# Kernel tuning notes

Hardware: AMD Instinct MI355X
Metric: run time of the kernel (lower is better)

## Reference

```python
import jax, jax.numpy as jnp
import numpy as np

B, S, E, H, D, W = 2, 4096, 512, 8, 64, 512
NUM_BUCKETS, MAX_DISTANCE = 32, 128  # hardcoded in get_relative_positions for 't5'
NEG_INF = -1e30


def _t5_bucket_causal(relative_position):
    """T5 relative position bucketing, unidirectional (causal)."""
    n = jnp.maximum(-relative_position, 0)
    max_exact = NUM_BUCKETS // 2
    is_small = n < max_exact
    nf = jnp.maximum(n.astype(jnp.float32), 1.0)
    val_if_large = max_exact + (
        jnp.log(nf / max_exact) / np.log(MAX_DISTANCE / max_exact)
        * (NUM_BUCKETS - max_exact)
    ).astype(jnp.int32)
    val_if_large = jnp.minimum(val_if_large, NUM_BUCKETS - 1)
    return jnp.where(is_small, n, val_if_large)


def setup_inputs() -> dict:
    key = jax.random.key(0)
    ks = jax.random.split(key, 7)
    scale = 1.0 / np.sqrt(E)  # keep logits in a sane range
    return {
        'xs': jax.random.normal(ks[0], (B, S, E), jnp.float32),
        'prev_k': jax.random.normal(ks[1], (B, W, H, D), jnp.float32),
        'prev_v': jax.random.normal(ks[2], (B, W, H, D), jnp.float32),
        'w_q': jax.random.normal(ks[3], (E, H, D), jnp.float32) * scale,
        'w_k': jax.random.normal(ks[4], (E, H, D), jnp.float32) * scale,
        'w_v': jax.random.normal(ks[5], (E, H, D), jnp.float32) * scale,
        'rel_bias': jax.random.normal(ks[6], (H, NUM_BUCKETS), jnp.float32),
    }


def reference(xs, prev_k, prev_v, w_q, w_k, w_v, rel_bias):
    nw = S // W  # number of windows
    # kvq projections; queries pre-scaled by 1/sqrt(head_size)
    q = jnp.einsum('bse,ehd->bshd', xs, w_q) * (1.0 / np.sqrt(D))
    k = jnp.einsum('bse,ehd->bshd', xs, w_k)
    v = jnp.einsum('bse,ehd->bshd', xs, w_v)
    qw = q.reshape(B, nw, W, H, D)
    kw = k.reshape(B, nw, W, H, D)
    vw = v.reshape(B, nw, W, H, D)
    # Transformer-XL sliding window: keys for window i = [window i-1 keys ; window i keys]
    k_prev = jnp.concatenate([prev_k[:, None], kw[:, :-1]], axis=1)  # (B,nw,W,H,D)
    v_prev = jnp.concatenate([prev_v[:, None], vw[:, :-1]], axis=1)
    k2 = jnp.concatenate([k_prev, kw], axis=2)  # (B,nw,2W,H,D)
    v2 = jnp.concatenate([v_prev, vw], axis=2)
    # T5 relative position bias and causal mask (num_queries=W, num_keys=2W)
    ctx = jnp.arange(W)[:, None] + W          # query absolute position in key frame
    mem = jnp.arange(2 * W)[None, :]
    relpos = mem - ctx                        # (W, 2W), key - query
    bias = rel_bias[:, _t5_bucket_causal(relpos)]  # (H, W, 2W)
    # causal + window mask: key j attends iff i < j <= i+W (each query sees exactly W keys)
    mask = (relpos <= 0) & (relpos > -W)
    # attention per window
    scores = jnp.einsum('bnqhd,bnkhd->bnhqk', qw, k2)  # (B,nw,H,W,2W)
    scores = scores + bias[None, None]
    scores = jnp.where(mask[None, None, None], scores, NEG_INF)
    probs = jax.nn.softmax(scores, axis=-1)
    attn = jnp.einsum('bnhqk,bnkhd->bnqhd', probs, v2)
    attn_ys = attn.reshape(B, S, H, D)
    # next_kvi cache = last window's keys/values
    next_k = kw[:, -1]
    next_v = vw[:, -1]
    return attn_ys, next_k, next_v
```

## Files before the change

### kernel.cpp

```cpp
#include <hip/hip_runtime.h>
#include <hip/hip_bf16.h>
#include <math.h>

#define B_ 2
#define S_ 4096
#define H_ 8
#define D_ 64
#define W_ 512

#define MASKV -1e30f

typedef float f32x4 __attribute__((ext_vector_type(4)));
typedef short s16x4 __attribute__((ext_vector_type(4)));
typedef short s16x8 __attribute__((ext_vector_type(8)));
typedef unsigned int u32;
typedef __attribute__((address_space(1))) const u32 as1_u32;
typedef __attribute__((address_space(3))) u32 as3_u32;

__device__ inline short f2bf(float f) {
    unsigned u = __builtin_bit_cast(unsigned, f);
    unsigned r = (u + 0x7FFFu + ((u >> 16) & 1u)) >> 16;
    return (short)r;
}
__device__ inline s16x8 pack8(f32x4 a, f32x4 b) {
    s16x8 r;
    r[0]=f2bf(a[0]); r[1]=f2bf(a[1]); r[2]=f2bf(a[2]); r[3]=f2bf(a[3]);
    r[4]=f2bf(b[0]); r[5]=f2bf(b[1]); r[6]=f2bf(b[2]); r[7]=f2bf(b[3]);
    return r;
}
__device__ __forceinline__ void gl_lds16(const void* g, void* l) {
    __builtin_amdgcn_global_load_lds((as1_u32*)(unsigned long long)g,
                                     (as3_u32*)(u32)(unsigned long long)l,
                                     16, 0, 0);
}
__device__ __forceinline__ void drain_vmem() {
    asm volatile("s_waitcnt vmcnt(0)" ::: "memory");
}

__global__ __launch_bounds__(256, 4)
void prep_kernel(const float* __restrict__ xs, const float* __restrict__ pk,
                 const float* __restrict__ pv, const float* __restrict__ wq,
                 const float* __restrict__ wk, const float* __restrict__ wv,
                 short* __restrict__ xsbf, short* __restrict__ pkbf,
                 short* __restrict__ vbt, short* __restrict__ wt)
{
    __shared__ char smem[17408];
    const int bid = blockIdx.x;
    const int tid = threadIdx.x;

    if (bid < 2304) {
        size_t i8 = ((size_t)bid * 256 + tid) * 8;
        const float* src; short* dst; size_t off;
        if (i8 < 4194304) { src = xs; dst = xsbf; off = i8; }
        else              { src = pk; dst = pkbf; off = i8 - 4194304; }
        f32x4 a = *(const f32x4*)(src + off);
        f32x4 b = *(const f32x4*)(src + off + 4);
        *(s16x8*)(dst + off) = pack8(a, b);
    } else if (bid < 2432) {
        short (*st)[72] = (short(*)[72])smem;
        const int b2 = bid - 2304;
        const int jt = b2 & 7, h = (b2 >> 3) & 7, b = b2 >> 6;
        const int jj0 = jt * 64;
        {
            int kk = tid >> 2, d0 = (tid & 3) * 16;
            const float* src = pv + (((size_t)(b * 512 + jj0 + kk)) * 8 + h) * 64 + d0;
            f32x4 x0 = *(const f32x4*)(src);
            f32x4 x1 = *(const f32x4*)(src + 4);
            f32x4 x2 = *(const f32x4*)(src + 8);
            f32x4 x3 = *(const f32x4*)(src + 12);
            *(s16x8*)&st[kk][d0]     = pack8(x0, x1);
            *(s16x8*)&st[kk][d0 + 8] = pack8(x2, x3);
        }
        __syncthreads();
        {
            int dd = tid >> 2, k0 = (tid & 3) * 16;
            s16x8 o0, o1;
            #pragma unroll
            for (int t = 0; t < 8; ++t) { o0[t] = st[k0 + t][dd]; o1[t] = st[k0 + 8 + t][dd]; }
            short* dst = vbt + (size_t)(h * 64 + dd) * 9216 + b * 4608 + jj0 + k0;
            *(s16x8*)dst = o0;
            *(s16x8*)(dst + 8) = o1;
        }
    } else {
        float (*st)[68] = (float(*)[68])smem;
        const int t2 = bid - 2432;
        const int k0 = (t2 & 7) * 64;
        const int nt = t2 >> 3;
        const int z  = nt >> 3;
        const int n0 = (nt & 7) * 64;
        const float* wz = (z == 0) ? wq : (z == 1) ? wk : wv;
        const float scale = (z == 0) ? 0.125f : 1.0f;
        {
            int kk = tid >> 4, nn = (tid & 15) * 4;
            #pragma unroll
            for (int it = 0; it < 4; ++it) {
                f32x4 x = *(const f32x4*)(wz + (size_t)(k0 + kk + it * 16) * 512 + n0 + nn);
                *(f32x4*)&st[kk + it * 16][nn] = x;
            }
        }
        __syncthreads();
        {
            int nn2 = tid >> 2, kseg = (tid & 3) * 16;
            s16x8 o0, o1;
            #pragma unroll
            for (int j = 0; j < 8; ++j) o0[j] = f2bf(st[kseg + j][nn2] * scale);
            #pragma unroll
            for (int j = 0; j < 8; ++j) o1[j] = f2bf(st[kseg + 8 + j][nn2] * scale);
            short* dst = wt + (size_t)(z * 512 + n0 + nn2) * 512 + k0 + kseg;
            *(s16x8*)(dst) = o0;
            *(s16x8*)(dst + 8) = o1;
        }
    }
}

__global__ __launch_bounds__(256, 4)
void proj_kernel(const short* __restrict__ xsbf, const short* __restrict__ wt,
                 short* __restrict__ qkbf, short* __restrict__ vbt,
                 float* __restrict__ out)
{
    __shared__ short Xs[128][64];
    __shared__ short Ws[128][64];

    const int tid = threadIdx.x;
    const int m0  = blockIdx.x * 128;
    const int n0  = blockIdx.y * 128;
    const int z   = n0 >> 9;
    const int ln0 = n0 & 511;
    const int wave = tid >> 6, lane = tid & 63;
    const int wq = (wave & 1) * 64;
    const int wx = (wave >> 1) * 64;
    const int lr = lane & 15, quad = lane >> 4;

    f32x4 acc[4][4] = {};

    const int r8  = lane >> 3;
    const int gr  = lane & 7;

    for (int k0 = 0; k0 < 512; k0 += 64) {
        #pragma unroll
        for (int i = 0; i < 4; ++i) {
            int row = 32 * wave + 8 * i + r8;
            int gs  = gr ^ (row & 7);
            gl_lds16(xsbf + (size_t)(m0 + row) * 512 + k0 + gs * 8, &Xs[32 * wave + 8 * i][0]);
            gl_lds16(wt   + (size_t)(n0 + row) * 512 + k0 + gs * 8, &Ws[32 * wave + 8 * i][0]);
        }
        drain_vmem();
        __syncthreads();
        #pragma unroll
        for (int ks = 0; ks < 2; ++ks) {
            s16x8 af[4], bf[4];
            #pragma unroll
            for (int ta = 0; ta < 4; ++ta) {
                int R = wq + ta * 16 + lr;
                af[ta] = *(const s16x8*)&Ws[R][(((ks * 4 + quad) ^ (R & 7)) * 8)];
            }
            #pragma unroll
            for (int tb = 0; tb < 4; ++tb) {
                int R = wx + tb * 16 + lr;
                bf[tb] = *(const s16x8*)&Xs[R][(((ks * 4 + quad) ^ (R & 7)) * 8)];
            }
            #pragma unroll
            for (int ta = 0; ta < 4; ++ta)
                #pragma unroll
                for (int tb = 0; tb < 4; ++tb)
                    acc[ta][tb] = __builtin_amdgcn_mfma_f32_16x16x32_bf16(
                        af[ta], bf[tb], acc[ta][tb], 0, 0, 0);
        }
        __syncthreads();
    }

    #pragma unroll
    for (int ta = 0; ta < 4; ++ta)
        #pragma unroll
        for (int tb = 0; tb < 4; ++tb) {
            int m  = m0 + wx + tb * 16 + lr;
            int ln = ln0 + wq + ta * 16 + quad * 4;
            int bb = m >> 12, seq = m & 4095;
            if (z < 2) {
                short* base = qkbf + (size_t)z * ((size_t)8192 * 512);
                s16x4 o;
                o[0] = f2bf(acc[ta][tb][0]); o[1] = f2bf(acc[ta][tb][1]);
                o[2] = f2bf(acc[ta][tb][2]); o[3] = f2bf(acc[ta][tb][3]);
                *(s16x4*)(base + (size_t)m * 512 + ln) = o;
                if (z == 1 && seq >= 3584) {
                    float* dst = out + 4194304 + ((size_t)(bb * 512 + seq - 3584)) * 512 + ln;
                    *(f32x4*)dst = acc[ta][tb];
                }
            } else {
                size_t col = (size_t)bb * 4608 + 512 + seq;
                #pragma unroll
                for (int g = 0; g < 4; ++g)
                    vbt[(size_t)(ln + g) * 9216 + col] = f2bf(acc[ta][tb][g]);
                if (seq >= 3584) {
                    float* dst = out + 4194304 + 524288 + ((size_t)(bb * 512 + seq - 3584)) * 512 + ln;
                    *(f32x4*)dst = acc[ta][tb];
                }
            }
        }
}

__global__ __launch_bounds__(512, 4)
void attn_kernel(const short* __restrict__ qkbf, const short* __restrict__ vbt,
                 const short* __restrict__ pkbf, const float* __restrict__ rel_bias,
                 float* __restrict__ out)
{
    __shared__ short k_s[2][64][64];
    __shared__ short vt_s[2][64][64];
    __shared__ short p_s[128][64];
    __shared__ float bias_s[512];

    const short* qb = qkbf;
    const short* kb = qkbf + (size_t)8192 * 512;

    const int bid = blockIdx.x;
    const int qt = bid & 3;
    const int h  = (bid >> 2) & 7;
    const int n  = (bid >> 5) & 7;
    const int b  = bid >> 8;
    const int tid = threadIdx.x;
    const int wave = tid >> 6, lane = tid & 63;
    const int lr = lane & 15, quad = lane >> 4;
    const int q0 = qt * 128;
    const int i0 = q0 + 16 * wave;

    {
        int nd = tid;
        int bucket;
        if (nd < 16) bucket = nd;
        else {
            int vbk = 16 + (int)(log((double)nd * (1.0 / 16.0)) * (16.0 / log(8.0)));
            bucket = vbk < 31 ? vbk : 31;
        }
        bias_s[nd] = rel_bias[h * 32 + bucket];
    }
    const float bias31 = rel_bias[h * 32 + 31];

    s16x8 aq[2];
    {
        const short* src = qb + (size_t)(b * S_ + n * W_ + i0 + lr) * 512 + h * 64 + quad * 8;
        aq[0] = *(const s16x8*)(src);
        aq[1] = *(const s16x8*)(src + 32);
    }

    f32x4 oacc[4] = {};
    float lsum = 0.f;

    const int cmin = (16 * wave) >> 6;
    const int cmax = (16 * wave + 527) >> 6;

    const int r8 = lane >> 3, gr = lane & 7;

    auto issueKV = [&](int c, int pb) {
        int jj = q0 + 64 * c + 8 * wave + r8;
        int p  = n * W_ + jj - W_;
        int gs = gr ^ r8;
        const short* ksrc = (p >= 0)
            ? kb   + ((size_t)(b * S_ + p)) * 512 + h * 64 + gs * 8
            : pkbf + (((size_t)(b * W_ + jj)) * 8 + h) * 64 + gs * 8;
        gl_lds16(ksrc, &k_s[pb][8 * wave][0]);
        int drow = 8 * wave + r8;
        const short* vsrc = vbt + (size_t)(h * 64 + drow) * 9216
                          + b * 4608 + n * W_ + q0 + 64 * c + gs * 8;
        gl_lds16(vsrc, &vt_s[pb][8 * wave][0]);
    };

    issueKV(0, 0);

    for (int c = 0; c < 10; ++c) {
        const int pb = c & 1;
        drain_vmem();
        __syncthreads();
        if (c < 9) issueKV(c + 1, pb ^ 1);
        if (c < cmin || c > cmax) continue;

        f32x4 sacc[4] = {};
        #pragma unroll
        for (int ks = 0; ks < 2; ++ks) {
            s16x8 bk[4];
            #pragma unroll
            for (int tn = 0; tn < 4; ++tn)
                bk[tn] = *(const s16x8*)&k_s[pb][tn * 16 + lr][(((4 * ks + quad) ^ (lr & 7)) * 8)];
            #pragma unroll
            for (int tn = 0; tn < 4; ++tn)
                sacc[tn] = __builtin_amdgcn_mfma_f32_16x16x32_bf16(
                    bk[tn], aq[ks], sacc[tn], 0, 0, 0);
        }

        const int ib = i0 + lr;
        const int jb = q0 + 64 * c;
        if (64 * c - 16 * wave <= 336) {
            #pragma unroll
            for (int tn = 0; tn < 4; ++tn) {
                s16x4 pp;
                #pragma unroll
                for (int rg = 0; rg < 4; ++rg) {
                    int j = jb + tn * 16 + quad * 4 + rg;
                    unsigned dm1 = (unsigned)(j - ib - 1);
                    float sv = (dm1 < 512u) ? (sacc[tn][rg] + bias31) : MASKV;
                    float p = __expf(sv);
                    lsum += p;
                    pp[rg] = f2bf(p);
                }
                int gp = (2 * tn + (quad >> 1)) ^ (lr & 7);
                *(s16x4*)&p_s[16 * wave + lr][gp * 8 + (quad & 1) * 4] = pp;
            }
        } else {
            #pragma unroll
            for (int tn = 0; tn < 4; ++tn) {
                s16x4 pp;
                #pragma unroll
                for (int rg = 0; rg < 4; ++rg) {
                    int j = jb + tn * 16 + quad * 4 + rg;
                    unsigned dm1 = (unsigned)(j - ib - 1);
                    float bias = bias_s[(ib + 512 - j) & 511];
                    float sv = (dm1 < 512u) ? (sacc[tn][rg] + bias) : MASKV;
                    float p = __expf(sv);
                    lsum += p;
                    pp[rg] = f2bf(p);
                }
                int gp = (2 * tn + (quad >> 1)) ^ (lr & 7);
                *(s16x4*)&p_s[16 * wave + lr][gp * 8 + (quad & 1) * 4] = pp;
            }
        }

        asm volatile("s_waitcnt lgkmcnt(0)" ::: "memory");

        #pragma unroll
        for (int ks = 0; ks < 2; ++ks) {
            int gpa = (4 * ks + quad) ^ (lr & 7);
            s16x8 ap = *(const s16x8*)&p_s[16 * wave + lr][gpa * 8];
            s16x8 bv[4];
            #pragma unroll
            for (int tn = 0; tn < 4; ++tn)
                bv[tn] = *(const s16x8*)&vt_s[pb][tn * 16 + lr][(((4 * ks + quad) ^ (lr & 7)) * 8)];
            #pragma unroll
            for (int tn = 0; tn < 4; ++tn)
                oacc[tn] = __builtin_amdgcn_mfma_f32_16x16x32_bf16(
                    ap, bv[tn], oacc[tn], 0, 0, 0);
        }
    }

    lsum += __shfl_xor(lsum, 16);
    lsum += __shfl_xor(lsum, 32);
    float linv[4];
    #pragma unroll
    for (int rg = 0; rg < 4; ++rg)
        linv[rg] = 1.0f / __shfl(lsum, quad * 4 + rg);

    #pragma unroll
    for (int rg = 0; rg < 4; ++rg) {
        int row = i0 + quad * 4 + rg;
        float* dst = out + (((size_t)b * S_ + n * W_ + row) * H_ + h) * D_ + lr;
        #pragma unroll
        for (int tn = 0; tn < 4; ++tn)
            dst[tn * 16] = oacc[tn][rg] * linv[rg];
    }
}

extern "C" void kernel_launch(void* const* d_in, const int* in_sizes, int n_in,
                              void* d_out, int out_size, void* d_ws, size_t ws_size,
                              hipStream_t stream)
{
    const float* xs       = (const float*)d_in[0];
    const float* prev_k   = (const float*)d_in[1];
    const float* prev_v   = (const float*)d_in[2];
    const float* w_q      = (const float*)d_in[3];
    const float* w_k      = (const float*)d_in[4];
    const float* w_v      = (const float*)d_in[5];
    const float* rel_bias = (const float*)d_in[6];
    float* out = (float*)d_out;

    short* xsbf = (short*)d_ws;
    short* wt   = xsbf + (size_t)4194304;
    short* qkbf = wt   + (size_t)786432;
    short* pkbf = qkbf + (size_t)8388608;
    short* vbt  = pkbf + (size_t)524288;

    prep_kernel<<<2624, 256, 0, stream>>>(xs, prev_k, prev_v, w_q, w_k, w_v,
                                          xsbf, pkbf, vbt, wt);

    proj_kernel<<<dim3(64, 12), 256, 0, stream>>>(xsbf, wt, qkbf, vbt, out);

    attn_kernel<<<512, 512, 0, stream>>>(qkbf, vbt, pkbf, rel_bias, out);
}
```

Before: 127.2 us.

## Double-buffer projection GEMM LDS tiles with K-step of 32

Splits the projection kernel's shared-memory tiles into two buffers with a K-step of 32 instead of 64. The next tile's global-to-LDS loads are issued right after the barrier so they overlap the current tile's MFMA work, and one of the two barriers per iteration is dropped. The cost is twice as many loop iterations and barriers, plus less MFMA work per wait, since drain_vmem still blocks at the top of each iteration.

```diff
diff --git a/kernel.cpp b/kernel.cpp
--- a/kernel.cpp
+++ b/kernel.cpp
@@ -118,8 +118,8 @@
                  short* __restrict__ qkbf, short* __restrict__ vbt,
                  float* __restrict__ out)
 {
-    __shared__ short Xs[128][64];
-    __shared__ short Ws[128][64];
+    __shared__ short Xs[2][128][32];
+    __shared__ short Ws[2][128][32];
 
     const int tid = threadIdx.x;
     const int m0  = blockIdx.x * 128;
@@ -133,40 +133,46 @@
 
     f32x4 acc[4][4] = {};
 
-    const int r8  = lane >> 3;
-    const int gr  = lane & 7;
-
-    for (int k0 = 0; k0 < 512; k0 += 64) {
-        #pragma unroll
-        for (int i = 0; i < 4; ++i) {
-            int row = 32 * wave + 8 * i + r8;
-            int gs  = gr ^ (row & 7);
-            gl_lds16(xsbf + (size_t)(m0 + row) * 512 + k0 + gs * 8, &Xs[32 * wave + 8 * i][0]);
-            gl_lds16(wt   + (size_t)(n0 + row) * 512 + k0 + gs * 8, &Ws[32 * wave + 8 * i][0]);
-        }
+    const int r16 = lane >> 2;
+    const int g4  = lane & 3;
+
+    auto issue = [&](int k0, int pb) {
+        #pragma unroll
+        for (int i = 0; i < 2; ++i) {
+            int row = 32 * wave + 16 * i + r16;
+            int gs  = g4 ^ (row & 3);
+            gl_lds16(xsbf + (size_t)(m0 + row) * 512 + k0 + gs * 8,
+                     &Xs[pb][32 * wave + 16 * i][0]);
+            gl_lds16(wt   + (size_t)(n0 + row) * 512 + k0 + gs * 8,
+                     &Ws[pb][32 * wave + 16 * i][0]);
+        }
+    };
+
+    issue(0, 0);
+
+    for (int it = 0; it < 16; ++it) {
+        const int pb = it & 1;
         drain_vmem();
         __syncthreads();
-        #pragma unroll
-        for (int ks = 0; ks < 2; ++ks) {
-            s16x8 af[4], bf[4];
-            #pragma unroll
-            for (int ta = 0; ta < 4; ++ta) {
-                int R = wq + ta * 16 + lr;
-                af[ta] = *(const s16x8*)&Ws[R][(((ks * 4 + quad) ^ (R & 7)) * 8)];
-            }
-            #pragma unroll
-            for (int tb = 0; tb < 4; ++tb) {
-                int R = wx + tb * 16 + lr;
-                bf[tb] = *(const s16x8*)&Xs[R][(((ks * 4 + quad) ^ (R & 7)) * 8)];
-            }
-            #pragma unroll
-            for (int ta = 0; ta < 4; ++ta)
-                #pragma unroll
-                for (int tb = 0; tb < 4; ++tb)
-                    acc[ta][tb] = __builtin_amdgcn_mfma_f32_16x16x32_bf16(
-                        af[ta], bf[tb], acc[ta][tb], 0, 0, 0);
-        }
-        __syncthreads();
+        if (it < 15) issue(32 * (it + 1), pb ^ 1);
+
+        s16x8 af[4], bf[4];
+        #pragma unroll
+        for (int ta = 0; ta < 4; ++ta) {
+            int R = wq + ta * 16 + lr;
+            af[ta] = *(const s16x8*)&Ws[pb][R][((quad ^ (R & 3)) * 8)];
+        }
+        #pragma unroll
+        for (int tb = 0; tb < 4; ++tb) {
+            int R = wx + tb * 16 + lr;
+            bf[tb] = *(const s16x8*)&Xs[pb][R][((quad ^ (R & 3)) * 8)];
+        }
+        #pragma unroll
+        for (int ta = 0; ta < 4; ++ta)
+            #pragma unroll
+            for (int tb = 0; tb < 4; ++tb)
+                acc[ta][tb] = __builtin_amdgcn_mfma_f32_16x16x32_bf16(
+                    af[ta], bf[tb], acc[ta][tb], 0, 0, 0);
     }
 
     #pragma unroll
```

Measured after the change: 132.1 us. 3.8% more time.
